# Optimization experiments

Measured on AMD Instinct MI355X. Metric: run time of the kernel, lower is better.

Reference implementation:

```python
import jax, jax.numpy as jnp
import numpy as np
from jax import lax

BIG = 1e30  # stand-in for +inf so gradients stay clean


def _cdist(pred, target):
    # pred: [B,N,3], target: [B,N,3] -> [B,N,N] Euclidean distances (torch.cdist p=2)
    diff = pred[:, :, None, :] - target[:, None, :, :]  # [B,N,N,3]
    return jnp.sqrt(jnp.sum(diff * diff, axis=-1))


def _greedy_match(cost):
    # cost: [N,N]; greedy row-by-row nearest unused target, matching the torch loop
    n = cost.shape[0]

    def step(used, row):
        masked = jnp.where(used, BIG, row)
        j = jnp.argmin(masked)
        c = masked[j]
        return used.at[j].set(True), c

    _, costs = lax.scan(step, jnp.zeros((n,), dtype=bool), cost)
    return jnp.sum(costs) / n


def setup_inputs() -> dict:
    key = jax.random.key(0)
    k1, k2 = jax.random.split(key)
    pred = jax.random.normal(k1, (8, 2048, 3), dtype=jnp.float32)
    target = jax.random.normal(k2, (8, 2048, 3), dtype=jnp.float32)
    return {"pred": pred, "target": target}


def reference(pred, target):
    cost = _cdist(pred, target)                 # [B,N,N]
    emd = jax.vmap(_greedy_match)(cost)         # [B]
    return jnp.mean(emd)
```

## Files before the change

kernel.cpp:

```cpp
#include <hip/hip_runtime.h>
#include <stdint.h>

#define N 2048
#define BATCH 8
#define NROWS (BATCH * N)
#define K64 64
#define LE 16
#define EXQ 2048
#define INV 0xFFFFFFFFu

typedef unsigned long long u64;
typedef unsigned u32;
typedef unsigned short u16;

#define DEADK 0xFFFFFFFFFFFFFFFFull

__device__ __forceinline__ unsigned wave_umin_bcast(unsigned x) {
#define DPP_MIN(ctrl)                                                          \
  {                                                                            \
    unsigned t = (unsigned)__builtin_amdgcn_update_dpp((int)x, (int)x, ctrl,   \
                                                       0xf, 0xf, false);       \
    x = t < x ? t : x;                                                         \
  }
  DPP_MIN(0x111) DPP_MIN(0x112) DPP_MIN(0x114) DPP_MIN(0x118)
  DPP_MIN(0x142) DPP_MIN(0x143)
#undef DPP_MIN
  return (unsigned)__builtin_amdgcn_readlane((int)x, 63);
}

__device__ __forceinline__ unsigned wave_umax_bcast(unsigned x) {
#define DPP_MAX(ctrl)                                                          \
  {                                                                            \
    unsigned t = (unsigned)__builtin_amdgcn_update_dpp((int)x, (int)x, ctrl,   \
                                                       0xf, 0xf, false);       \
    x = t > x ? t : x;                                                         \
  }
  DPP_MAX(0x111) DPP_MAX(0x112) DPP_MAX(0x114) DPP_MAX(0x118)
  DPP_MAX(0x142) DPP_MAX(0x143)
#undef DPP_MAX
  return (unsigned)__builtin_amdgcn_readlane((int)x, 63);
}

#define DPP64_MIN(x, ctrl)                                                     \
  {                                                                            \
    u32 lo_ = (u32)(x), hi_ = (u32)((x) >> 32);                                \
    u32 tlo_ = (u32)__builtin_amdgcn_update_dpp((int)lo_, (int)lo_, (ctrl),    \
                                                0xf, 0xf, false);              \
    u32 thi_ = (u32)__builtin_amdgcn_update_dpp((int)hi_, (int)hi_, (ctrl),    \
                                                0xf, 0xf, false);              \
    u64 t_ = ((u64)thi_ << 32) | tlo_;                                         \
    x = t_ < x ? t_ : x;                                                       \
  }

__device__ __forceinline__ u64 wave_min64_l63(u64 x) {
  DPP64_MIN(x, 0x111) DPP64_MIN(x, 0x112) DPP64_MIN(x, 0x114)
  DPP64_MIN(x, 0x118) DPP64_MIN(x, 0x142) DPP64_MIN(x, 0x143)
  return x;
}

#define DIST(qx, qy, qz, TX, TY, TZ, j, dout)                                  \
  do {                                                                         \
    _Pragma("clang fp contract(off)")                                          \
    float dx_ = (qx) - (TX)[j];                                                \
    float dy_ = (qy) - (TY)[j];                                                \
    float dz_ = (qz) - (TZ)[j];                                                \
    float s_ = dx_ * dx_ + dy_ * dy_ + dz_ * dz_;                              \
    dout = sqrtf(s_);                                                          \
  } while (0)

__global__ __launch_bounds__(256, 1)
void emd_shortsort_kernel(const float* __restrict__ pred,
                          const float* __restrict__ target,
                          u64* __restrict__ keys) {
    __shared__ float tx[N], ty[N], tz[N];
    __shared__ u64 cand[4 * 256];

    const int b  = blockIdx.x >> 9;
    const int r0 = (blockIdx.x & 511) << 2;
    const float* tb = target + (size_t)b * N * 3;

    for (int idx = threadIdx.x; idx < 3 * N; idx += 256) {
        float v = tb[idx];
        int n = idx / 3, c = idx - 3 * n;
        if (c == 0) tx[n] = v; else if (c == 1) ty[n] = v; else tz[n] = v;
    }
    __syncthreads();

    const int wid = threadIdx.x >> 6, lane = threadIdx.x & 63;
    const int i = r0 + wid;
    const size_t row = (size_t)b * N + i;
    const float* pb = pred + row * 3;
    const float qx = pb[0], qy = pb[1], qz = pb[2];

    float d[32];
    float m = 3.4e38f;
    #pragma unroll
    for (int c = 0; c < 32; ++c) {
        const int j = (c << 6) + lane;
        float dd;
        DIST(qx, qy, qz, tx, ty, tz, j, dd);
        d[c] = dd;
        m = fminf(m, dd);
    }

    unsigned mb = __float_as_uint(m);
    {
        unsigned t = (unsigned)__builtin_amdgcn_update_dpp((int)mb, (int)mb,
                                                           0x0B1, 0xf, 0xf, false);
        mb = t < mb ? t : mb;
    }
    const unsigned tau = wave_umax_bcast(mb);
    const float tauf = __uint_as_float(tau);

    u64* cw = cand + wid * 256;
    unsigned base = 0;
    #pragma unroll
    for (int c = 0; c < 32; ++c) {
        const bool p = d[c] <= tauf;
        const u64 bm = __ballot(p);
        if (p) {
            unsigned off = base + (unsigned)__popcll(bm & ((1ull << lane) - 1ull));
            if (off < 256u)
                cw[off] = ((u64)__float_as_uint(d[c]) << 32) |
                          (unsigned)((c << 6) + lane);
        }
        base += (unsigned)__popcll(bm);
    }
    const u32 lim = (base > 256u) ? 0u : base;

    u64 k0 = ((u32)lane       < lim) ? cw[lane      ] : DEADK;
    u64 k1 = ((u32)lane + 64  < lim) ? cw[lane + 64 ] : DEADK;
    u64 k2 = ((u32)lane + 128 < lim) ? cw[lane + 128] : DEADK;
    u64 k3 = ((u32)lane + 192 < lim) ? cw[lane + 192] : DEADK;

#define CSWAP(a, b)                                                            \
  { u64 mn_ = (a) < (b) ? (a) : (b); u64 mx_ = (a) < (b) ? (b) : (a);          \
    (a) = mn_; (b) = mx_; }
    CSWAP(k0, k1) CSWAP(k2, k3) CSWAP(k0, k2) CSWAP(k1, k3) CSWAP(k1, k2)
#undef CSWAP

    u64 mykey = DEADK;
    for (int it = 0; it < K64; ++it) {
        u64 wm = wave_min64_l63(k0);
        u32 wlo = (u32)__builtin_amdgcn_readlane((int)(u32)wm, 63);
        u32 whi = (u32)__builtin_amdgcn_readlane((int)(u32)(wm >> 32), 63);
        if (whi == 0xFFFFFFFFu) break;
        const u64 wkey = ((u64)whi << 32) | wlo;
        mykey = (lane == it) ? wkey : mykey;
        const bool eq = (k0 == wkey);
        k0 = eq ? k1 : k0; k1 = eq ? k2 : k1; k2 = eq ? k3 : k2;
        k3 = eq ? DEADK : k3;
    }
    keys[row * (size_t)K64 + lane] = mykey;
}

#define SEG_PROBE(LISTBASE, SEG, R)                                            \
    const uint4 w_ = *(const uint4*)&(LISTBASE)[(SEG)];                        \
    const u32 t0_ = w_.x & 0xFFFFu, t1_ = w_.x >> 16;                          \
    const u32 t2_ = w_.y & 0xFFFFu, t3_ = w_.y >> 16;                          \
    const u32 t4_ = w_.z & 0xFFFFu, t5_ = w_.z >> 16;                          \
    const u32 t6_ = w_.w & 0xFFFFu, t7_ = w_.w >> 16;                          \
    const u32 h0_ = holder[t0_ & (N - 1)], h1_ = holder[t1_ & (N - 1)];        \
    const u32 h2_ = holder[t2_ & (N - 1)], h3_ = holder[t3_ & (N - 1)];        \
    const u32 h4_ = holder[t4_ & (N - 1)], h5_ = holder[t5_ & (N - 1)];        \
    const u32 h6_ = holder[t6_ & (N - 1)], h7_ = holder[t7_ & (N - 1)];        \
    u32 am_ = 0, dm_ = 0;                                                      \
    if (t0_ == 0xFFFFu) dm_ |= 1u;   else if (h0_ > (R)) am_ |= 1u;            \
    if (t1_ == 0xFFFFu) dm_ |= 2u;   else if (h1_ > (R)) am_ |= 2u;            \
    if (t2_ == 0xFFFFu) dm_ |= 4u;   else if (h2_ > (R)) am_ |= 4u;            \
    if (t3_ == 0xFFFFu) dm_ |= 8u;   else if (h3_ > (R)) am_ |= 8u;            \
    if (t4_ == 0xFFFFu) dm_ |= 16u;  else if (h4_ > (R)) am_ |= 16u;           \
    if (t5_ == 0xFFFFu) dm_ |= 32u;  else if (h5_ > (R)) am_ |= 32u;           \
    if (t6_ == 0xFFFFu) dm_ |= 64u;  else if (h6_ > (R)) am_ |= 64u;           \
    if (t7_ == 0xFFFFu) dm_ |= 128u; else if (h7_ > (R)) am_ |= 128u;

#define SEG_TARGET(E)                                                          \
    ((E) < 2 ? ((E) & 1 ? t1_ : t0_)                                           \
             : (E) < 4 ? ((E) & 1 ? t3_ : t2_)                                 \
                       : (E) < 6 ? ((E) & 1 ? t5_ : t4_)                       \
                                 : ((E) & 1 ? t7_ : t6_))

__global__ __launch_bounds__(1024, 1)
void emd_da9_kernel(const float* __restrict__ pred,
                    const float* __restrict__ target,
                    const u64* __restrict__ keys,
                    float* __restrict__ batch_emd) {
    __shared__ float tx[N], ty[N], tz[N];
    __shared__ float px[N], py[N], pz[N];
    __shared__ u32 holder[N];
    __shared__ u16 posn[N];
    __shared__ u16 list16[N * LE];
    __shared__ u16 exq[EXQ];
    __shared__ u32 talloc, head;
    __shared__ double dsum[1024];

    const int tid = threadIdx.x;
    const int lane = tid & 63;
    const int b = blockIdx.x;
    const float* pb = pred + (size_t)b * N * 3;
    const float* tb = target + (size_t)b * N * 3;
    const u64* kb = keys + (size_t)b * N * (size_t)K64;

    for (int idx = tid; idx < 3 * N; idx += 1024) {
        float vp = pb[idx], vt = tb[idx];
        int n = idx / 3, c = idx - 3 * n;
        if (c == 0)      { px[n] = vp; tx[n] = vt; }
        else if (c == 1) { py[n] = vp; ty[n] = vt; }
        else             { pz[n] = vp; tz[n] = vt; }
    }
    for (int j = tid; j < N; j += 1024) { holder[j] = INV; posn[j] = 0; }
    if (tid == 0) { talloc = 0; head = 0; }
    for (int idx = tid; idx < N * LE; idx += 1024) {
        const int row = idx >> 4, e = idx & (LE - 1);
        const u64 key = kb[(size_t)row * K64 + e];
        list16[idx] = ((u32)(key >> 32) == INV) ? (u16)0xFFFF
                                                : (u16)((u32)key & (N - 1));
    }
    __syncthreads();

    #pragma unroll
    for (int k = 0; k < 2; ++k) {
        u32 r = (u32)tid + (k ? 1024u : 0u);
        u32 p = 0;
        for (int guard = 0; guard < 200000; ++guard) {
            if (p >= LE) {
                posn[r] = LE;
                const u32 s = atomicAdd(&talloc, 1u);
                exq[s & (EXQ - 1)] = (u16)r;
                break;
            }
            const u32 seg = p & ~7u;
            SEG_PROBE(list16 + (r << 4), seg, r)
            const u32 lv = 0xFFu & ~((1u << (p - seg)) - 1u);
            const u32 evm = (am_ | dm_) & lv;
            if (!evm) { p = seg + 8; continue; }
            const u32 e = (u32)__builtin_ctz(evm);
            if (dm_ & (1u << e)) {
                posn[r] = 64;
                const u32 s = atomicAdd(&talloc, 1u);
                exq[s & (EXQ - 1)] = (u16)r;
                break;
            }
            const u32 t = SEG_TARGET(e);
            const u32 old = atomicMin(&holder[t], r);
            if (old < r) { p = seg + e + 1; continue; }
            posn[r] = (u16)(seg + e + 1);
            if (old == INV) break;
            r = old; p = (u32)posn[r];
        }
    }
    __syncthreads();

    {
        const u32 TA = talloc;
        for (int guard = 0; guard < 20000; ++guard) {
            u32 i = 0;
            if (lane == 0) i = atomicAdd(&head, 1u);
            i = (u32)__builtin_amdgcn_readlane((int)i, 0);
            if (i >= TA) break;
            u32 r = (u32)exq[i & (EXQ - 1)];

            for (int cg = 0; cg < 200000; ++cg) {
                u32 p = (u32)posn[r];
                u32 nextr = INV;
                bool matched_free = false, resolved = false;

                for (int w8 = 0; w8 < 24 && !resolved; ++w8) {
                    if (p >= LE) break;
                    const u32 seg = p & ~7u;
                    SEG_PROBE(list16 + (r << 4), seg, r)
                    const u32 lv = 0xFFu & ~((1u << (p - seg)) - 1u);
                    const u32 evm = (am_ | dm_) & lv;
                    if (!evm) { p = seg + 8; continue; }
                    const u32 e = (u32)__builtin_ctz(evm);
                    if (dm_ & (1u << e)) { p = 64; break; }
                    const u32 t = SEG_TARGET(e);
                    u32 old = 0;
                    if (lane == 0) old = atomicMin(&holder[t], r);
                    old = (u32)__builtin_amdgcn_readlane((int)old, 0);
                    if (old < r) { p = seg + e + 1; continue; }
                    if (lane == 0) posn[r] = (u16)(seg + e + 1);
                    resolved = true;
                    if (old == INV) matched_free = true; else nextr = old;
                }
                if (!resolved && lane == 0) posn[r] = (u16)p;

                if (!resolved && p < 64) {
                    const u64 key = kb[(size_t)r * K64 + lane];
                    const u32 dv = (u32)(key >> 32);
                    const u32 t = (u32)key & (N - 1);
                    const bool cand = ((u32)lane >= p) && (dv != INV) &&
                                      (holder[t] > r);
                    u64 bal = __ballot(cand);
                    while (bal) {
                        const int L = __ffsll((long long)bal) - 1;
                        const u32 tL = (u32)__builtin_amdgcn_readlane((int)t, L);
                        u32 old = 0;
                        if (lane == 0) old = atomicMin(&holder[tL], r);
                        old = (u32)__builtin_amdgcn_readlane((int)old, 0);
                        if (old > r) {
                            if (lane == 0) posn[r] = (u16)(L + 1);
                            resolved = true;
                            if (old == INV) matched_free = true;
                            else nextr = old;
                            break;
                        }
                        bal &= ~(1ull << (u32)L);
                    }
                }

                if (!resolved) {
                    const float qx = px[r], qy = py[r], qz = pz[r];
                    u32 dbits[32];
                    #pragma unroll
                    for (int c = 0; c < 32; ++c) {
                        const int j = (c << 6) + lane;
                        float dd;
                        DIST(qx, qy, qz, tx, ty, tz, j, dd);
                        dbits[c] = __float_as_uint(dd);
                    }
                    for (int rty = 0; rty < 100000; ++rty) {
                        u64 best = DEADK;
                        #pragma unroll 8
                        for (int c = 0; c < 32; ++c) {
                            const int j = (c << 6) + lane;
                            if (holder[j] > r) {
                                const u64 kk = ((u64)dbits[c] << 32) | (u32)j;
                                if (kk < best) best = kk;
                            }
                        }
                        const u64 wm = wave_min64_l63(best);
                        const u32 jw =
                            (u32)__builtin_amdgcn_readlane((int)(u32)wm, 63) &
                            (N - 1);
                        u32 old = 0;
                        if (lane == 0) old = atomicMin(&holder[jw], r);
                        old = (u32)__builtin_amdgcn_readlane((int)old, 0);
                        if (old < r) continue;
                        if (lane == 0) posn[r] = 64;
                        if (old == INV) matched_free = true; else nextr = old;
                        break;
                    }
                }

                if (matched_free) break;
                r = nextr;
            }
        }
    }
    __syncthreads();

    double s = 0.0;
    #pragma unroll
    for (int k = 0; k < 2; ++k) {
        const int t = tid + (k ? 1024 : 0);
        const u32 r = holder[t] & (N - 1);
        float dd;
        DIST(px[r], py[r], pz[r], tx, ty, tz, t, dd);
        s += (double)dd;
    }
    dsum[tid] = s;
    __syncthreads();
    for (int st = 512; st >= 1; st >>= 1) {
        if (tid < st) dsum[tid] += dsum[tid + st];
        __syncthreads();
    }
    if (tid == 0) batch_emd[b] = (float)(dsum[0] / N);
}

__device__ __forceinline__ u64 full_scan_row(
    int lane, float qx, float qy, float qz,
    const float* tx, const float* ty, const float* tz,
    const unsigned char* used) {
  u32 dl = 0xFFFFFFFFu, jl = 0u;
  #pragma unroll 8
  for (int c = 0; c < 32; ++c) {
    const int j = (c << 6) + lane;
    if (!used[j]) {
      float dd;
      DIST(qx, qy, qz, tx, ty, tz, j, dd);
      const u32 db = __float_as_uint(dd);
      if (db < dl) { dl = db; jl = (u32)j; }
    }
  }
  const u32 dmin = wave_umin_bcast(dl);
  const u32 jc = (dl == dmin) ? jl : 0xFFFFFFFFu;
  const u32 jmin = wave_umin_bcast(jc);
  return ((u64)dmin << 32) | jmin;
}

__global__ __launch_bounds__(64, 1)
void emd_greedy_full_kernel(const float* __restrict__ pred,
                            const float* __restrict__ target,
                            float* __restrict__ batch_emd) {
    __shared__ float tx[N], ty[N], tz[N];
    __shared__ float qxs[N], qys[N], qzs[N];
    __shared__ unsigned char used[N];

    const int lane = threadIdx.x;
    const int b = blockIdx.x;
    const float* pb = pred + (size_t)b * N * 3;
    const float* tb = target + (size_t)b * N * 3;

    for (int idx = lane; idx < 3 * N; idx += 64) {
        float vp = pb[idx], vt = tb[idx];
        int n = idx / 3, c = idx - 3 * n;
        if (c == 0)      { qxs[n] = vp; tx[n] = vt; }
        else if (c == 1) { qys[n] = vp; ty[n] = vt; }
        else             { qzs[n] = vp; tz[n] = vt; }
    }
    for (int j = lane; j < N; j += 64) used[j] = 0;

    double sum = 0.0;
    for (int i = 0; i < N; ++i) {
        u64 fs = full_scan_row(lane, qxs[i], qys[i], qzs[i], tx, ty, tz, used);
        sum += (double)__uint_as_float((u32)(fs >> 32));
        if (lane == 0) used[(u32)fs] = 1;
    }
    if (lane == 0) batch_emd[b] = (float)(sum / N);
}

__global__ void emd_mean_kernel(const float* __restrict__ batch_emd,
                                float* __restrict__ out) {
    double s = 0.0;
    for (int b = 0; b < BATCH; ++b) s += (double)batch_emd[b];
    out[0] = (float)(s / BATCH);
}

extern "C" void kernel_launch(void* const* d_in, const int* in_sizes, int n_in,
                              void* d_out, int out_size, void* d_ws, size_t ws_size,
                              hipStream_t stream) {
    const float* pred   = (const float*)d_in[0];
    const float* target = (const float*)d_in[1];
    float* out = (float*)d_out;
    char* wsb = (char*)d_ws;

    const size_t keysz = (size_t)NROWS * K64 * 8;
    if (ws_size >= keysz + 64) {
        u64* keys = (u64*)wsb;
        float* emd = (float*)(wsb + keysz);
        emd_shortsort_kernel<<<NROWS / 4, 256, 0, stream>>>(pred, target, keys);
        emd_da9_kernel<<<BATCH, 1024, 0, stream>>>(pred, target, keys, emd);
        emd_mean_kernel<<<1, 1, 0, stream>>>(emd, out);
    } else {
        float* emd = (float*)wsb;
        emd_greedy_full_kernel<<<BATCH, 64, 0, stream>>>(pred, target, emd);
        emd_mean_kernel<<<1, 1, 0, stream>>>(emd, out);
    }
}
```

Measured before the change: 526.4 us.

## Cache extended candidate lists in LDS pool and use wave-shuffle final reduction

Rows whose first 16 candidates are exhausted now get an LDS slot from a bounded pool. The pool holds candidates 16..63 as u16 target indices, so later probes use the segmented LDS probe instead of re-reading 64-bit keys from global memory and ballot-scanning them. When the pool is full, rows fall back to the old global-memory ballot path. The final per-block sum switches from a 10-step LDS tree with barriers to wave shuffles plus a 16-entry sum. This adds LDS usage and more branching in the matching loop.

```diff
diff --git a/kernel.cpp b/kernel.cpp
--- a/kernel.cpp
+++ b/kernel.cpp
@@ -7,6 +7,7 @@
 #define K64 64
 #define LE 16
 #define EXQ 2048
+#define ESLOTS 288
 #define INV 0xFFFFFFFFu
 
 typedef unsigned long long u64;
@@ -181,18 +182,20 @@
                                  : ((E) & 1 ? t7_ : t6_))
 
 __global__ __launch_bounds__(1024, 1)
-void emd_da9_kernel(const float* __restrict__ pred,
-                    const float* __restrict__ target,
-                    const u64* __restrict__ keys,
-                    float* __restrict__ batch_emd) {
+void emd_da11_kernel(const float* __restrict__ pred,
+                     const float* __restrict__ target,
+                     const u64* __restrict__ keys,
+                     float* __restrict__ batch_emd) {
     __shared__ float tx[N], ty[N], tz[N];
     __shared__ float px[N], py[N], pz[N];
     __shared__ u32 holder[N];
     __shared__ u16 posn[N];
     __shared__ u16 list16[N * LE];
+    __shared__ u16 extslot[N];
+    __shared__ u16 extpool[ESLOTS * 48];
     __shared__ u16 exq[EXQ];
-    __shared__ u32 talloc, head;
-    __shared__ double dsum[1024];
+    __shared__ u32 talloc, head, ealloc;
+    __shared__ double dsum[16];
 
     const int tid = threadIdx.x;
     const int lane = tid & 63;
@@ -208,8 +211,10 @@
         else if (c == 1) { py[n] = vp; ty[n] = vt; }
         else             { pz[n] = vp; tz[n] = vt; }
     }
-    for (int j = tid; j < N; j += 1024) { holder[j] = INV; posn[j] = 0; }
-    if (tid == 0) { talloc = 0; head = 0; }
+    for (int j = tid; j < N; j += 1024) {
+        holder[j] = INV; posn[j] = 0; extslot[j] = 0xFFFF;
+    }
+    if (tid == 0) { talloc = 0; head = 0; ealloc = 0; }
     for (int idx = tid; idx < N * LE; idx += 1024) {
         const int row = idx >> 4, e = idx & (LE - 1);
         const u64 key = kb[(size_t)row * K64 + e];
@@ -265,7 +270,7 @@
                 u32 nextr = INV;
                 bool matched_free = false, resolved = false;
 
-                for (int w8 = 0; w8 < 24 && !resolved; ++w8) {
+                for (int w8 = 0; w8 < 8 && !resolved; ++w8) {
                     if (p >= LE) break;
                     const u32 seg = p & ~7u;
                     SEG_PROBE(list16 + (r << 4), seg, r)
@@ -283,29 +288,72 @@
                     resolved = true;
                     if (old == INV) matched_free = true; else nextr = old;
                 }
-                if (!resolved && lane == 0) posn[r] = (u16)p;
-
-                if (!resolved && p < 64) {
-                    const u64 key = kb[(size_t)r * K64 + lane];
-                    const u32 dv = (u32)(key >> 32);
-                    const u32 t = (u32)key & (N - 1);
-                    const bool cand = ((u32)lane >= p) && (dv != INV) &&
-                                      (holder[t] > r);
-                    u64 bal = __ballot(cand);
-                    while (bal) {
-                        const int L = __ffsll((long long)bal) - 1;
-                        const u32 tL = (u32)__builtin_amdgcn_readlane((int)t, L);
-                        u32 old = 0;
-                        if (lane == 0) old = atomicMin(&holder[tL], r);
-                        old = (u32)__builtin_amdgcn_readlane((int)old, 0);
-                        if (old > r) {
-                            if (lane == 0) posn[r] = (u16)(L + 1);
+
+                if (!resolved && p >= LE && p < 64) {
+                    u32 sl = (u32)extslot[r];
+                    if (sl == 0xFFFFu) {
+                        u32 ns = 0;
+                        if (lane == 0) ns = atomicAdd(&ealloc, 1u);
+                        ns = (u32)__builtin_amdgcn_readlane((int)ns, 0);
+                        if (ns < (u32)ESLOTS) {
+                            if (lane >= 16) {
+                                const u64 key = kb[(size_t)r * K64 + lane];
+                                extpool[ns * 48 + (lane - 16)] =
+                                    ((u32)(key >> 32) == INV)
+                                        ? (u16)0xFFFF
+                                        : (u16)((u32)key & (N - 1));
+                            }
+                            if (lane == 0) extslot[r] = (u16)ns;
+                            sl = ns;
+                        }
+                    }
+                    if (sl < (u32)ESLOTS) {
+                        for (int w8 = 0; w8 < 8 && !resolved; ++w8) {
+                            if (p >= 64) break;
+                            const u32 ei = p - LE;
+                            const u32 seg = ei & ~7u;
+                            SEG_PROBE(extpool + sl * 48, seg, r)
+                            const u32 lv = 0xFFu & ~((1u << (ei - seg)) - 1u);
+                            const u32 evm = (am_ | dm_) & lv;
+                            if (!evm) { p = LE + seg + 8; continue; }
+                            const u32 e = (u32)__builtin_ctz(evm);
+                            if (dm_ & (1u << e)) { p = 64; break; }
+                            const u32 t = SEG_TARGET(e);
+                            u32 old = 0;
+                            if (lane == 0) old = atomicMin(&holder[t], r);
+                            old = (u32)__builtin_amdgcn_readlane((int)old, 0);
+                            if (old < r) { p = LE + seg + e + 1; continue; }
+                            if (lane == 0) posn[r] = (u16)(LE + seg + e + 1);
                             resolved = true;
                             if (old == INV) matched_free = true;
                             else nextr = old;
-                            break;
                         }
-                        bal &= ~(1ull << (u32)L);
+                        if (!resolved && lane == 0) posn[r] = (u16)p;
+                    } else {
+                        const u64 key = kb[(size_t)r * K64 + lane];
+                        const u32 dv = (u32)(key >> 32);
+                        const u32 t = (u32)key & (N - 1);
+                        const bool cand = ((u32)lane >= p) && (dv != INV) &&
+                                          (holder[t] > r);
+                        u64 bal = __ballot(cand);
+                        while (bal) {
+                            const int L = __ffsll((long long)bal) - 1;
+                            const u32 tL =
+                                (u32)__builtin_amdgcn_readlane((int)t, L);
+                            u32 old = 0;
+                            if (lane == 0) old = atomicMin(&holder[tL], r);
+                            old = (u32)__builtin_amdgcn_readlane((int)old, 0);
+                            if (old > r) {
+                                if (lane == 0) posn[r] = (u16)(L + 1);
+                                resolved = true;
+                                if (old == INV) matched_free = true;
+                                else nextr = old;
+                                break;
+                            }
+                            bal &= ~(1ull << (u32)L);
+                        }
+                        if (!resolved && lane == 0) posn[r] = 64;
+                        if (!resolved) p = 64;
                     }
                 }
 
@@ -359,13 +407,16 @@
         DIST(px[r], py[r], pz[r], tx, ty, tz, t, dd);
         s += (double)dd;
     }
-    dsum[tid] = s;
+    #pragma unroll
+    for (int m = 32; m >= 1; m >>= 1) s += __shfl_down(s, m, 64);
+    if (lane == 0) dsum[tid >> 6] = s;
     __syncthreads();
-    for (int st = 512; st >= 1; st >>= 1) {
-        if (tid < st) dsum[tid] += dsum[tid + st];
-        __syncthreads();
-    }
-    if (tid == 0) batch_emd[b] = (float)(dsum[0] / N);
+    if (tid == 0) {
+        double tot = 0.0;
+        #pragma unroll
+        for (int w = 0; w < 16; ++w) tot += dsum[w];
+        batch_emd[b] = (float)(tot / N);
+    }
 }
 
 __device__ __forceinline__ u64 full_scan_row(
@@ -440,7 +491,7 @@
         u64* keys = (u64*)wsb;
         float* emd = (float*)(wsb + keysz);
         emd_shortsort_kernel<<<NROWS / 4, 256, 0, stream>>>(pred, target, keys);
-        emd_da9_kernel<<<BATCH, 1024, 0, stream>>>(pred, target, keys, emd);
+        emd_da11_kernel<<<BATCH, 1024, 0, stream>>>(pred, target, keys, emd);
         emd_mean_kernel<<<1, 1, 0, stream>>>(emd, out);
     } else {
         float* emd = (float*)wsb;
```

After: 588.2 us. 1.12x slower.
